# Performance work log

Measured on AMD Instinct MI355X. Metric: run time of the kernel, lower is better.

## Reference

```python
import jax, jax.numpy as jnp
import numpy as np

N_NODES = 50000      # both nbr (src) and agent (dst) node counts
DEG = 16             # fixed in-degree per agent for the synthetic graph
MAX_NBRS = 32        # args.max_nbrs
NBR_IN, AGENT_IN, HID, NBR_OUT, AGENT_OUT = 128, 128, 128, 8, 8


def setup_inputs() -> dict:
    key = jax.random.key(0)
    ks = jax.random.split(key, 8)
    E = N_NODES * DEG
    # Edges sorted by destination agent; slot = position within agent's nbr list
    edge_dst = jnp.repeat(jnp.arange(N_NODES, dtype=jnp.int64), DEG)
    edge_slot = jnp.tile(jnp.arange(DEG, dtype=jnp.int64), N_NODES)
    edge_src = jax.random.randint(ks[0], (E,), 0, N_NODES, dtype=jnp.int64)
    scale1 = 1.0 / np.sqrt(NBR_IN + AGENT_IN)
    scale2 = 1.0 / np.sqrt(HID)
    return {
        "x_nbr": jax.random.normal(ks[1], (N_NODES, NBR_IN), dtype=jnp.float32),
        "x_agent": jax.random.normal(ks[2], (N_NODES, AGENT_IN), dtype=jnp.float32),
        "W1": jax.random.normal(ks[3], (NBR_IN + AGENT_IN, HID), dtype=jnp.float32) * scale1,
        "b1": jnp.zeros((HID,), dtype=jnp.float32),
        "W2": jax.random.normal(ks[4], (HID, NBR_OUT), dtype=jnp.float32) * scale2,
        "b2": jnp.zeros((NBR_OUT,), dtype=jnp.float32),
        "Wa": jax.random.normal(ks[5], (AGENT_IN, AGENT_OUT), dtype=jnp.float32) * scale2,
        "ba": jnp.zeros((AGENT_OUT,), dtype=jnp.float32),
        "edge_src": edge_src,
        "edge_dst": edge_dst,
        "edge_slot": edge_slot,
    }


def reference(x_nbr, x_agent, W1, b1, W2, b2, Wa, ba, edge_src, edge_dst, edge_slot):
    n_agents = x_agent.shape[0]
    # apply_edges: gather src/dst features per edge, cat, 2-layer MLP -> score
    h = jnp.concatenate([x_nbr[edge_src], x_agent[edge_dst]], axis=1)  # [E, 256]
    scores = jax.nn.relu(h @ W1 + b1) @ W2 + b2                        # [E, NBR_OUT]
    # ragged split + zero-pad to max_nbrs, expressed as a dense scatter
    padded = jnp.zeros((n_agents, MAX_NBRS, NBR_OUT), dtype=scores.dtype)
    padded = padded.at[edge_dst, edge_slot].set(scores)
    padded = padded.reshape(n_agents, MAX_NBRS * NBR_OUT)              # [N, 256]
    own_score = x_agent @ Wa + ba                                      # [N, AGENT_OUT]
    return jnp.concatenate([padded, own_score], axis=1)                # [N, 264]
```

## Files before the change

kernel.cpp:

```cpp
#include <hip/hip_runtime.h>

typedef unsigned int u32;
typedef unsigned short u16;
typedef __attribute__((ext_vector_type(2))) float f32x2;
typedef __attribute__((ext_vector_type(4))) float f32x4;
typedef __attribute__((ext_vector_type(8))) __bf16 bf16x8;
typedef __attribute__((ext_vector_type(4))) u32 u32x4;

__device__ __forceinline__ u32 f2bf(float f) {
    u32 u = __builtin_bit_cast(u32, f);
    return (u + 0x7fffu + ((u >> 16) & 1u)) >> 16;
}
__device__ __forceinline__ u32 pk2(float lo, float hi) {
    return f2bf(lo) | (f2bf(hi) << 16);
}
__device__ __forceinline__ float bflo(u32 a) { return __builtin_bit_cast(float, a << 16); }
__device__ __forceinline__ float bfhi(u32 a) { return __builtin_bit_cast(float, a & 0xffff0000u); }

union LdsTile {
    u16 h[16 * 136];
    u32x4 v[16 * 17];
};

__global__ __launch_bounds__(256, 2)
void precompute_kernel(const float* __restrict__ x_nbr,
                       const float* __restrict__ x_agent,
                       const float* __restrict__ W1,
                       const float* __restrict__ b1,
                       const float* __restrict__ Wa,
                       const float* __restrict__ ba,
                       u16* __restrict__ np, u16* __restrict__ ap,
                       float* __restrict__ out,
                       int n_nodes, int n_agents, int nbr_blocks)
{
    __shared__ LdsTile Abuf[4];
    const int wid = threadIdx.x >> 6;
    const int l   = threadIdx.x & 63;
    const int n   = l & 15;
    const int q   = l >> 4;
    const bool is_nbr = (int)blockIdx.x < nbr_blocks;

    const float* Wb = W1 + (is_nbr ? 0 : 128 * 128);
    u32x4 wf[8][4];
#pragma unroll
    for (int nt = 0; nt < 8; ++nt) {
        const int col = nt * 16 + n;
#pragma unroll
        for (int kk = 0; kk < 4; ++kk) {
            u32x4 w;
#pragma unroll
            for (int jp = 0; jp < 4; ++jp) {
                const int k = kk * 32 + q * 8 + jp * 2;
                w[jp] = pk2(Wb[(size_t)k * 128 + col], Wb[(size_t)(k + 1) * 128 + col]);
            }
            wf[nt][kk] = w;
        }
    }
    const f32x4 zero = {0.f, 0.f, 0.f, 0.f};

    if (is_nbr) {
        const int n_tiles = n_nodes >> 4;
        const int gw = blockIdx.x * 4 + wid;
        const int stride = nbr_blocks * 4;
        for (int t = gw; t < n_tiles; t += stride) {
            const int a0 = t * 16;
#pragma unroll
            for (int it = 0; it < 4; ++it) {
                const int m = it * 4 + q;
                const float* bp = x_nbr + (size_t)(a0 + m) * 128 + n * 8;
                const float4 v0 = *(const float4*)bp;
                const float4 v1 = *(const float4*)(bp + 4);
                u32x4 pkv;
                pkv[0] = pk2(v0.x, v0.y); pkv[1] = pk2(v0.z, v0.w);
                pkv[2] = pk2(v1.x, v1.y); pkv[3] = pk2(v1.z, v1.w);
                Abuf[wid].v[m * 17 + n] = pkv;
            }
            f32x4 acc[8];
#pragma unroll
            for (int nt = 0; nt < 8; ++nt) acc[nt] = zero;
#pragma unroll
            for (int kk = 0; kk < 4; ++kk) {
                const u32x4 a = Abuf[wid].v[n * 17 + kk * 4 + q];
#pragma unroll
                for (int nt = 0; nt < 8; ++nt)
                    acc[nt] = __builtin_amdgcn_mfma_f32_16x16x32_bf16(
                        __builtin_bit_cast(bf16x8, a),
                        __builtin_bit_cast(bf16x8, wf[nt][kk]), acc[nt], 0, 0, 0);
            }
#pragma unroll
            for (int nt = 0; nt < 8; ++nt)
#pragma unroll
                for (int r = 0; r < 4; ++r)
                    np[(size_t)(a0 + q * 4 + r) * 128 + nt * 16 + n] =
                        (u16)f2bf(acc[nt][r]);
        }
    } else {
        u32x4 waf[4];
#pragma unroll
        for (int kk = 0; kk < 4; ++kk) {
            u32x4 w;
#pragma unroll
            for (int jp = 0; jp < 4; ++jp) {
                const int k = kk * 32 + q * 8 + jp * 2;
                const float f0 = (n < 8) ? Wa[(size_t)k * 8 + n] : 0.f;
                const float f1 = (n < 8) ? Wa[(size_t)(k + 1) * 8 + n] : 0.f;
                w[jp] = pk2(f0, f1);
            }
            waf[kk] = w;
        }
        float b1v[8];
#pragma unroll
        for (int nt = 0; nt < 8; ++nt) b1v[nt] = b1[nt * 16 + n];
        const float bav = (n < 8) ? ba[n] : 0.f;

        const int n_tiles = n_agents >> 4;
        const int agent_blocks = gridDim.x - nbr_blocks;
        const int gw = (blockIdx.x - nbr_blocks) * 4 + wid;
        const int stride = agent_blocks * 4;
        for (int t = gw; t < n_tiles; t += stride) {
            const int a0 = t * 16;
#pragma unroll
            for (int it = 0; it < 4; ++it) {
                const int m = it * 4 + q;
                const float* bp = x_agent + (size_t)(a0 + m) * 128 + n * 8;
                const float4 v0 = *(const float4*)bp;
                const float4 v1 = *(const float4*)(bp + 4);
                u32x4 pkv;
                pkv[0] = pk2(v0.x, v0.y); pkv[1] = pk2(v0.z, v0.w);
                pkv[2] = pk2(v1.x, v1.y); pkv[3] = pk2(v1.z, v1.w);
                Abuf[wid].v[m * 17 + n] = pkv;
            }
            f32x4 acc[8];
#pragma unroll
            for (int nt = 0; nt < 8; ++nt) acc[nt] = zero;
            f32x4 acca = zero;
#pragma unroll
            for (int kk = 0; kk < 4; ++kk) {
                const u32x4 a = Abuf[wid].v[n * 17 + kk * 4 + q];
#pragma unroll
                for (int nt = 0; nt < 8; ++nt)
                    acc[nt] = __builtin_amdgcn_mfma_f32_16x16x32_bf16(
                        __builtin_bit_cast(bf16x8, a),
                        __builtin_bit_cast(bf16x8, wf[nt][kk]), acc[nt], 0, 0, 0);
                acca = __builtin_amdgcn_mfma_f32_16x16x32_bf16(
                    __builtin_bit_cast(bf16x8, a),
                    __builtin_bit_cast(bf16x8, waf[kk]), acca, 0, 0, 0);
            }
#pragma unroll
            for (int nt = 0; nt < 8; ++nt)
#pragma unroll
                for (int r = 0; r < 4; ++r)
                    ap[(size_t)(a0 + q * 4 + r) * 128 + nt * 16 + n] =
                        (u16)f2bf(acc[nt][r] + b1v[nt]);
            const float4 z = {0.f, 0.f, 0.f, 0.f};
#pragma unroll
            for (int it = 0; it < 4; ++it) {
                const int m = it * 4 + q;
                float4* zp = (float4*)(out + (size_t)(a0 + m) * 264 + 128 + n * 8);
                zp[0] = z; zp[1] = z;
            }
#pragma unroll
            for (int r = 0; r < 4; ++r) {
                const int m = q * 4 + r;
                if (n < 8) out[(size_t)(a0 + m) * 264 + 256 + n] = acca[r] + bav;
            }
        }
    }
}

struct GSet { u32x4 np[4]; u32x4 ap[4]; };

__device__ __forceinline__ void async_idx(const int* p, int& v) {
    asm volatile("global_load_dword %0, %1, off" : "=v"(v) : "v"(p) : "memory");
}
__device__ __forceinline__ void issue_block(const u16* npb, const u16* apb, GSet& g) {
    asm volatile(
        "global_load_dwordx4 %0, %8, off sc0\n\t"
        "global_load_dwordx4 %1, %9, off sc0\n\t"
        "global_load_dwordx4 %2, %8, off offset:64 sc0\n\t"
        "global_load_dwordx4 %3, %9, off offset:64 sc0\n\t"
        "global_load_dwordx4 %4, %8, off offset:128 sc0\n\t"
        "global_load_dwordx4 %5, %9, off offset:128 sc0\n\t"
        "global_load_dwordx4 %6, %8, off offset:192 sc0\n\t"
        "global_load_dwordx4 %7, %9, off offset:192 sc0"
        : "=&v"(g.np[0]), "=&v"(g.ap[0]), "=&v"(g.np[1]), "=&v"(g.ap[1]),
          "=&v"(g.np[2]), "=&v"(g.ap[2]), "=&v"(g.np[3]), "=&v"(g.ap[3])
        : "v"(npb), "v"(apb) : "memory");
}
__device__ __forceinline__ void issue_gathers(const u16* __restrict__ np,
                                              const u16* __restrict__ ap,
                                              int src_self, int t, int q, GSet& g)
{
    issue_block(np + (size_t)(unsigned)src_self * 128 + q * 8,
                ap + (size_t)(unsigned)t        * 128 + q * 8, g);
}

#define WAITP_(N, a, b) \
    asm volatile("s_waitcnt vmcnt(" #N ")" : "+v"(a), "+v"(b) :: "memory")
#define WAITP(N, a, b) WAITP_(N, a, b)

__device__ __forceinline__ u32 relu_pk(u32 av, u32 bv) {
    f32x2 a = {bflo(av), bfhi(av)};
    f32x2 b = {bflo(bv), bfhi(bv)};
    const f32x2 s = a + b;
    const float lo = fmaxf(s[0], 0.f);
    const float hi = fmaxf(s[1], 0.f);
    u32 r;
    asm("v_cvt_pk_bf16_f32 %0, %1, %2" : "=v"(r) : "v"(lo), "v"(hi));
    return r;
}
__device__ __forceinline__ u32x4 relu_pk4(const u32x4& a, const u32x4& b) {
    u32x4 hf;
    hf[0] = relu_pk(a[0], b[0]); hf[1] = relu_pk(a[1], b[1]);
    hf[2] = relu_pk(a[2], b[2]); hf[3] = relu_pk(a[3], b[3]);
    return hf;
}

#define MFMA_BF16(A, B, C) __builtin_amdgcn_mfma_f32_16x16x32_bf16( \
    __builtin_bit_cast(bf16x8, A), __builtin_bit_cast(bf16x8, B), (C), 0, 0, 0)

#define COMPUTE_TILE(G, DST, W0, W1N, W2N, W3N) do {                          \
    f32x4 acc2 = {0.f, 0.f, 0.f, 0.f};                                        \
    WAITP(W0,  (G).np[0], (G).ap[0]);                                         \
    acc2 = MFMA_BF16(relu_pk4((G).np[0], (G).ap[0]), w2f[0], acc2);           \
    WAITP(W1N, (G).np[1], (G).ap[1]);                                         \
    acc2 = MFMA_BF16(relu_pk4((G).np[1], (G).ap[1]), w2f[1], acc2);           \
    WAITP(W2N, (G).np[2], (G).ap[2]);                                         \
    acc2 = MFMA_BF16(relu_pk4((G).np[2], (G).ap[2]), w2f[2], acc2);           \
    WAITP(W3N, (G).np[3], (G).ap[3]);                                         \
    acc2 = MFMA_BF16(relu_pk4((G).np[3], (G).ap[3]), w2f[3], acc2);           \
    float* orow = out + (size_t)(DST) * 264;                                  \
    _Pragma("unroll")                                                         \
    for (int r = 0; r < 4; ++r)                                               \
        if (n < 8) orow[(q * 4 + r) * 8 + n] = acc2[r] + b2v;                 \
} while (0)

template<int PC>
__device__ __forceinline__ void pipe_step(const u16* __restrict__ np,
                                          const u16* __restrict__ ap,
                                          const int* __restrict__ edge_src,
                                          float* __restrict__ out,
                                          int t_c, int t_f, int t_a,
                                          int q, int n,
                                          int (&sreg)[2], GSet (&g)[2],
                                          const u32x4 (&w2f)[4], float b2v)
{
    constexpr int PF = 1 - PC;
    async_idx(edge_src + (size_t)t_a * 16 + n, sreg[PC]);
    asm volatile("s_waitcnt vmcnt(13)" : "+v"(sreg[PF]) :: "memory");
    issue_gathers(np, ap, sreg[PF], t_f, q, g[PF]);
    COMPUTE_TILE(g[PC], t_c, 19, 17, 15, 13);
}

__global__ __launch_bounds__(256, 3)
void edge_kernel(const u16* __restrict__ np, const u16* __restrict__ ap,
                 const float* __restrict__ W2, const float* __restrict__ b2,
                 const int* __restrict__ edge_src,
                 float* __restrict__ out, int n_tiles)
{
    const int wid = threadIdx.x >> 6;
    const int l   = threadIdx.x & 63;
    const int n   = l & 15;
    const int q   = l >> 4;

    u32x4 w2f[4];
#pragma unroll
    for (int kk = 0; kk < 4; ++kk) {
        u32x4 w;
#pragma unroll
        for (int jp = 0; jp < 4; ++jp) {
            const int k = kk * 32 + q * 8 + jp * 2;
            const float f0 = (n < 8) ? W2[(size_t)k * 8 + n] : 0.f;
            const float f1 = (n < 8) ? W2[(size_t)(k + 1) * 8 + n] : 0.f;
            w[jp] = pk2(f0, f1);
        }
        w2f[kk] = w;
    }
    const float b2v = (n < 8) ? b2[n] : 0.f;

    const int stride = gridDim.x * 4;
    const int gw = blockIdx.x * 4 + wid;
    if (gw >= n_tiles) return;
    const int nt_w = (n_tiles - gw + stride - 1) / stride;

    int t_c = gw;
    int t_f = (t_c + stride < n_tiles) ? t_c + stride : t_c;
    int t_a = (t_f + stride < n_tiles) ? t_f + stride : t_f;

    int sreg[2];
    GSet g[2];

    async_idx(edge_src + (size_t)t_c * 16 + n, sreg[0]);
    async_idx(edge_src + (size_t)t_f * 16 + n, sreg[1]);
    asm volatile("s_waitcnt vmcnt(0)" : "+v"(sreg[0]), "+v"(sreg[1]) :: "memory");
    issue_gathers(np, ap, sreg[0], t_c, q, g[0]);
    async_idx(edge_src + (size_t)t_a * 16 + n, sreg[0]);
    issue_gathers(np, ap, sreg[1], t_f, q, g[1]);
    COMPUTE_TILE(g[0], t_c, 15, 13, 11, 9);

    int i = 1;
    while (true) {
        if (i >= nt_w) break;
        t_c = t_f; t_f = t_a;
        t_a = (t_a + stride < n_tiles) ? t_a + stride : t_a;
        pipe_step<1>(np, ap, edge_src, out, t_c, t_f, t_a,
                     q, n, sreg, g, w2f, b2v);
        if (++i >= nt_w) break;
        t_c = t_f; t_f = t_a;
        t_a = (t_a + stride < n_tiles) ? t_a + stride : t_a;
        pipe_step<0>(np, ap, edge_src, out, t_c, t_f, t_a,
                     q, n, sreg, g, w2f, b2v);
        ++i;
    }
}

extern "C" void kernel_launch(void* const* d_in, const int* in_sizes, int n_in,
                              void* d_out, int out_size, void* d_ws, size_t ws_size,
                              hipStream_t stream)
{
    const float* x_nbr   = (const float*)d_in[0];
    const float* x_agent = (const float*)d_in[1];
    const float* W1      = (const float*)d_in[2];
    const float* b1      = (const float*)d_in[3];
    const float* W2      = (const float*)d_in[4];
    const float* b2      = (const float*)d_in[5];
    const float* Wa      = (const float*)d_in[6];
    const float* ba      = (const float*)d_in[7];
    const int* edge_src  = (const int*)d_in[8];

    const int E        = in_sizes[8];
    const int n_nodes  = in_sizes[0] / 128;
    const int n_agents = in_sizes[1] / 128;
    const int n_tiles  = E / 16;

    u16* np = (u16*)d_ws;
    u16* ap = (u16*)d_ws + (size_t)n_nodes * 128;

    const int nbr_blocks = 512, agent_blocks = 512;
    precompute_kernel<<<dim3(nbr_blocks + agent_blocks), dim3(256), 0, stream>>>(
        x_nbr, x_agent, W1, b1, Wa, ba, np, ap, (float*)d_out,
        n_nodes, n_agents, nbr_blocks);
    edge_kernel<<<dim3(768), dim3(256), 0, stream>>>(
        np, ap, W2, b2, edge_src, (float*)d_out, n_tiles);
}
```

Baseline: 171.2 us.

## Stage W1 bf16 fragments in LDS instead of registers in precompute kernel

New measurement: 199.9 us. 1.17x slower.

```diff
diff --git a/kernel.cpp b/kernel.cpp
--- a/kernel.cpp
+++ b/kernel.cpp
@@ -22,7 +22,7 @@
     u32x4 v[16 * 17];
 };
 
-__global__ __launch_bounds__(256, 2)
+__global__ __launch_bounds__(256, 3)
 void precompute_kernel(const float* __restrict__ x_nbr,
                        const float* __restrict__ x_agent,
                        const float* __restrict__ W1,
@@ -34,6 +34,7 @@
                        int n_nodes, int n_agents, int nbr_blocks)
 {
     __shared__ LdsTile Abuf[4];
+    __shared__ u32x4 wfrag[8][4][4][16];
     const int wid = threadIdx.x >> 6;
     const int l   = threadIdx.x & 63;
     const int n   = l & 15;
@@ -41,21 +42,22 @@
     const bool is_nbr = (int)blockIdx.x < nbr_blocks;
 
     const float* Wb = W1 + (is_nbr ? 0 : 128 * 128);
-    u32x4 wf[8][4];
-#pragma unroll
-    for (int nt = 0; nt < 8; ++nt) {
-        const int col = nt * 16 + n;
-#pragma unroll
-        for (int kk = 0; kk < 4; ++kk) {
-            u32x4 w;
-#pragma unroll
-            for (int jp = 0; jp < 4; ++jp) {
-                const int k = kk * 32 + q * 8 + jp * 2;
-                w[jp] = pk2(Wb[(size_t)k * 128 + col], Wb[(size_t)(k + 1) * 128 + col]);
-            }
-            wf[nt][kk] = w;
+
+    {
+        const int tid  = threadIdx.x;
+        const int c    = tid & 127;
+        const int half = tid >> 7;
+#pragma unroll 4
+        for (int it = 0; it < 32; ++it) {
+            const int rp = it * 2 + half;
+            const int k  = rp * 2;
+            const float f0 = Wb[(size_t)k * 128 + c];
+            const float f1 = Wb[(size_t)(k + 1) * 128 + c];
+            wfrag[c >> 4][rp >> 4][(rp >> 2) & 3][c & 15][rp & 3] = pk2(f0, f1);
         }
     }
+    __syncthreads();
+
     const f32x4 zero = {0.f, 0.f, 0.f, 0.f};
 
     if (is_nbr) {
@@ -81,11 +83,14 @@
 #pragma unroll
             for (int kk = 0; kk < 4; ++kk) {
                 const u32x4 a = Abuf[wid].v[n * 17 + kk * 4 + q];
+                u32x4 wv[8];
+#pragma unroll
+                for (int nt = 0; nt < 8; ++nt) wv[nt] = wfrag[nt][kk][q][n];
 #pragma unroll
                 for (int nt = 0; nt < 8; ++nt)
                     acc[nt] = __builtin_amdgcn_mfma_f32_16x16x32_bf16(
                         __builtin_bit_cast(bf16x8, a),
-                        __builtin_bit_cast(bf16x8, wf[nt][kk]), acc[nt], 0, 0, 0);
+                        __builtin_bit_cast(bf16x8, wv[nt]), acc[nt], 0, 0, 0);
             }
 #pragma unroll
             for (int nt = 0; nt < 8; ++nt)
@@ -137,11 +142,14 @@
 #pragma unroll
             for (int kk = 0; kk < 4; ++kk) {
                 const u32x4 a = Abuf[wid].v[n * 17 + kk * 4 + q];
+                u32x4 wv[8];
+#pragma unroll
+                for (int nt = 0; nt < 8; ++nt) wv[nt] = wfrag[nt][kk][q][n];
 #pragma unroll
                 for (int nt = 0; nt < 8; ++nt)
                     acc[nt] = __builtin_amdgcn_mfma_f32_16x16x32_bf16(
                         __builtin_bit_cast(bf16x8, a),
-                        __builtin_bit_cast(bf16x8, wf[nt][kk]), acc[nt], 0, 0, 0);
+                        __builtin_bit_cast(bf16x8, wv[nt]), acc[nt], 0, 0, 0);
                 acca = __builtin_amdgcn_mfma_f32_16x16x32_bf16(
                     __builtin_bit_cast(bf16x8, a),
                     __builtin_bit_cast(bf16x8, waf[kk]), acca, 0, 0, 0);
@@ -336,7 +344,7 @@
     u16* np = (u16*)d_ws;
     u16* ap = (u16*)d_ws + (size_t)n_nodes * 128;
 
-    const int nbr_blocks = 512, agent_blocks = 512;
+    const int nbr_blocks = 384, agent_blocks = 384;
     precompute_kernel<<<dim3(nbr_blocks + agent_blocks), dim3(256), 0, stream>>>(
         x_nbr, x_agent, W1, b1, Wa, ba, np, ap, (float*)d_out,
         n_nodes, n_agents, nbr_blocks);
```
